# Optimization experiments

Hardware: AMD Instinct MI355X
Metric: run time of the kernel (lower is better)

The kernel has to match this reference:

```python
import jax, jax.numpy as jnp
import numpy as np

B, T, C, HEAD = 4, 4096, 1024, 64

def _rope_tables(t, d):
    # standard RoPE angles; each frequency repeated for the (even, odd) pair
    inv_freq = 1.0 / (10000.0 ** (np.arange(0, d, 2, dtype=np.float32) / d))  # (d/2,)
    ang = np.arange(t, dtype=np.float32)[:, None] * inv_freq[None, :]          # (t, d/2)
    ang = np.repeat(ang, 2, axis=-1)                                           # (t, d)
    return jnp.asarray(np.cos(ang)), jnp.asarray(np.sin(ang))

def setup_inputs() -> dict:
    key = jax.random.key(0)
    kx, kq, kk, kv = jax.random.split(key, 4)
    cos, sin = _rope_tables(T, HEAD)
    s = 1.0 / np.sqrt(C)
    return {
        "x": jax.random.normal(kx, (B, T, C), dtype=jnp.float32),
        "cos": cos,
        "sin": sin,
        "tril": jnp.tril(jnp.ones((T, T), dtype=jnp.int32)),
        "Wq": jax.random.normal(kq, (C, HEAD), dtype=jnp.float32) * s,
        "Wk": jax.random.normal(kk, (C, HEAD), dtype=jnp.float32) * s,
        "Wv": jax.random.normal(kv, (C, HEAD), dtype=jnp.float32) * s,
    }

def _apply_rope(x, cos, sin):
    # x: (B, T, D); cos/sin: (T, D)
    x1 = x[..., ::2]
    x2 = x[..., 1::2]
    rot = jnp.stack([-x2, x1], axis=-1).reshape(x.shape)
    return x * cos[None] + rot * sin[None]

def reference(x, cos, sin, tril, Wq, Wk, Wv):
    q = _apply_rope(x @ Wq, cos, sin)          # (B, T, D)
    k = _apply_rope(x @ Wk, cos, sin)          # (B, T, D)
    v = x @ Wv                                  # (B, T, D)
    scale = HEAD ** -0.5
    wei = jnp.einsum("btd,bsd->bts", q, k) * scale   # (B, T, T)
    wei = jnp.where(tril[None] == 0, -jnp.inf, wei)
    wei = jax.nn.softmax(wei, axis=-1)               # dropout p=0 (eval) -> identity
    return jnp.einsum("bts,bsd->btd", wei, v)        # (B, T, D)
```

## Files before the change

### kernel.cpp

```cpp
#include <hip/hip_runtime.h>
#include <math.h>

#define T_ 4096
#define NROWS 16384

typedef __attribute__((ext_vector_type(8))) short short8;
typedef __attribute__((ext_vector_type(4))) short short4v;
typedef __attribute__((ext_vector_type(4))) float float4v;
typedef __attribute__((ext_vector_type(2))) unsigned uint2v;

#define MFMA(a, b, c) __builtin_amdgcn_mfma_f32_16x16x32_bf16((a), (b), (c), 0, 0, 0)

#if defined(__has_builtin)
#if __has_builtin(__builtin_amdgcn_exp2f)
#define EXP2(x) __builtin_amdgcn_exp2f(x)
#else
#define EXP2(x) exp2f(x)
#endif
#else
#define EXP2(x) exp2f(x)
#endif

#define SCALE_Q 0.18033688011112042f

__device__ __forceinline__ short f2bf(float f) {
    unsigned u = __builtin_bit_cast(unsigned, f);
    u += 0x7fffu + ((u >> 16) & 1u);
    return (short)(u >> 16);
}
__device__ __forceinline__ float bf2f(short s) {
    return __builtin_bit_cast(float, ((unsigned)(unsigned short)s) << 16);
}
__device__ __forceinline__ unsigned pack_bf2(float a, float b) {
    unsigned ua = __builtin_bit_cast(unsigned, a);
    unsigned ub = __builtin_bit_cast(unsigned, b);
    ua += 0x7fffu + ((ua >> 16) & 1u);
    ub += 0x7fffu + ((ub >> 16) & 1u);
    return (ua >> 16) | (ub & 0xffff0000u);
}

__global__ void wprep_kernel(const float* __restrict__ Wq,
                             const float* __restrict__ Wk,
                             const float* __restrict__ Wv,
                             short* __restrict__ Wt2)
{
    const int ck = blockIdx.x;
    const int t = threadIdx.x;
    const int sub = t >> 6, lane = t & 63;
    const int ln = lane & 15, quad = lane >> 4;
#pragma unroll
    for (int jj = 0; jj < 3; ++jj) {
        const int nt = sub * 3 + jj;
        const float* W = (nt < 4) ? Wq : (nt < 8) ? Wk : Wv;
        const int col = (nt & 3) * 16 + ln;
        short8 o;
#pragma unroll
        for (int j = 0; j < 8; ++j)
            o[j] = f2bf(W[(size_t)(ck * 32 + quad * 8 + j) * 64 + col]);
        *(short8*)(Wt2 + ((size_t)(ck * 12 + nt) * 64 + lane) * 8) = o;
    }
}

__global__ __launch_bounds__(256, 2) void qkv_kernel(
    const float* __restrict__ x, const float* __restrict__ cosp,
    const float* __restrict__ sinp, const short* __restrict__ Wt2,
    short* __restrict__ Qb, short* __restrict__ Ks, short* __restrict__ Vs)
{
    __shared__ short4v MB[4][2][12][64];
    __shared__ short KT[32][72];

    const int t = threadIdx.x, w = t >> 6, lane = t & 63;
    const int ln = lane & 15, quad = lane >> 4;
    const int rb = blockIdx.x * 32;
    const int k0 = w * 256;

    const float* xp0 = x + (size_t)(rb + ln) * 1024 + k0 + quad * 8;
    const float* xp1 = x + (size_t)(rb + 16 + ln) * 1024 + k0 + quad * 8;
    const short* wp2 = Wt2 + ((size_t)(w * 8) * 12 * 64 + lane) * 8;

    short8 a[2][8];
#pragma unroll
    for (int af = 0; af < 2; ++af) {
        const float* xp = af ? xp1 : xp0;
        float4 xf[16];
#pragma unroll
        for (int it = 0; it < 8; ++it) {
            xf[it * 2]     = *(const float4*)(xp + it * 32);
            xf[it * 2 + 1] = *(const float4*)(xp + it * 32 + 4);
        }
#pragma unroll
        for (int it = 0; it < 8; ++it) {
            short8 v;
            v[0] = f2bf(xf[it * 2].x);     v[1] = f2bf(xf[it * 2].y);
            v[2] = f2bf(xf[it * 2].z);     v[3] = f2bf(xf[it * 2].w);
            v[4] = f2bf(xf[it * 2 + 1].x); v[5] = f2bf(xf[it * 2 + 1].y);
            v[6] = f2bf(xf[it * 2 + 1].z); v[7] = f2bf(xf[it * 2 + 1].w);
            a[af][it] = v;
        }
    }

    float4v acc[2][12];
#pragma unroll
    for (int af = 0; af < 2; ++af)
#pragma unroll
        for (int i = 0; i < 12; ++i) acc[af][i] = (float4v){0.f, 0.f, 0.f, 0.f};

#pragma unroll
    for (int it = 0; it < 8; ++it) {
        short8 bf[12];
#pragma unroll
        for (int nt = 0; nt < 12; ++nt)
            bf[nt] = *(const short8*)(wp2 + (size_t)(it * 12 + nt) * 512);
#pragma unroll
        for (int nt = 0; nt < 12; ++nt) {
            acc[0][nt] = MFMA(a[0][it], bf[nt], acc[0][nt]);
            acc[1][nt] = MFMA(a[1][it], bf[nt], acc[1][nt]);
        }
    }

#pragma unroll
    for (int af = 0; af < 2; ++af)
#pragma unroll
        for (int nt = 0; nt < 12; ++nt) {
            short4v pv;
#pragma unroll
            for (int reg = 0; reg < 4; ++reg) pv[reg] = f2bf(acc[af][nt][reg]);
            MB[w][af][nt][lane] = pv;
        }
    __syncthreads();

    const int b  = rb >> 12;
    const int kt = (rb & (T_ - 1)) >> 6;
#pragma unroll
    for (int af = 0; af < 2; ++af) {
        const int rb16 = rb + af * 16;
#pragma unroll
        for (int j = 0; j < 3; ++j) {
            const int nt = w * 3 + j;
            float m[4] = {0.f, 0.f, 0.f, 0.f};
#pragma unroll
            for (int p = 0; p < 4; ++p) {
                const short4v pv = MB[p][af][nt][lane];
#pragma unroll
                for (int reg = 0; reg < 4; ++reg) m[reg] += bf2f(pv[reg]);
            }
            if (nt < 4) {
                const int col = nt * 16 + ln;
#pragma unroll
                for (int reg = 0; reg < 4; ++reg) {
                    const int g  = rb16 + quad * 4 + reg;
                    const int tp = g & (T_ - 1);
                    const float cv = cosp[(size_t)tp * 64 + col];
                    const float sv = sinp[(size_t)tp * 64 + col];
                    const float v  = m[reg];
                    const float vp = __shfl_xor(v, 1, 64);
                    const float rot = (ln & 1) ? vp : -vp;
                    Qb[(size_t)g * 64 + col] = f2bf(fmaf(v, cv, rot * sv) * SCALE_Q);
                }
            } else if (nt < 8) {
                const int col = (nt & 3) * 16 + ln;
#pragma unroll
                for (int reg = 0; reg < 4; ++reg) {
                    const int g  = rb16 + quad * 4 + reg;
                    const int tp = g & (T_ - 1);
                    const float cv = cosp[(size_t)tp * 64 + col];
                    const float sv = sinp[(size_t)tp * 64 + col];
                    const float v  = m[reg];
                    const float vp = __shfl_xor(v, 1, 64);
                    const float rot = (ln & 1) ? vp : -vp;
                    KT[af * 16 + quad * 4 + reg][col] = f2bf(fmaf(v, cv, rot * sv));
                }
            } else {
                const int vnt = nt - 8;
                const int rowgrp = (rb16 >> 4) & 3;
                const int hh = rowgrp >> 1;
                const int qp = (rowgrp & 1) * 2 + (quad >> 1);
                const int jb = (quad & 1) * 4;
                short4v pv;
#pragma unroll
                for (int reg = 0; reg < 4; ++reg) pv[reg] = f2bf(m[reg]);
                const size_t addr =
                    ((((size_t)(b * 64 + kt) * 4 + vnt) * 2 + hh) * 64 + qp * 16 + ln) * 8 + jb;
                *(short4v*)(Vs + addr) = pv;
            }
        }
    }
    __syncthreads();

    {
        const int af2 = w >> 1, h2 = w & 1;
        const int st2 = ((rb >> 4) & 3) + af2;
        const short8 kfrag = *(const short8*)(&KT[af2 * 16 + ln][h2 * 32 + quad * 8]);
        *(short8*)(Ks + (((size_t)(b * 64 + kt) * 8 + st2 * 2 + h2) * 64 + lane) * 8) = kfrag;
    }
}

#define LOADK(kf, ktv)                                                         \
    {   const short* _kb = Ksp + (size_t)(ktv) * 4096 + lane * 8;              \
        _Pragma("unroll")                                                      \
        for (int u = 0; u < 8; ++u) kf[u] = *(const short8*)(_kb + u * 512); }

#define LOADV(vf, ktv)                                                         \
    {   const short* _vb = Vp + (size_t)(ktv) * 4096 + lane * 8;               \
        _Pragma("unroll")                                                      \
        for (int u = 0; u < 8; ++u) vf[u] = *(const short8*)(_vb + u * 512); }

#define STEP(ktv, kf, vf, masked)                                              \
    {   float4v s[4];                                                          \
        _Pragma("unroll")                                                      \
        for (int st = 0; st < 4; ++st) {                                       \
            s[st] = (float4v){0.f, 0.f, 0.f, 0.f};                             \
            s[st] = MFMA(kf[st * 2],     qb0, s[st]);         \
            s[st] = MFMA(kf[st * 2 + 1], qb1, s[st]);                          \
        }                                                                      \
        if (masked) {                                                          \
            _Pragma("unroll")                                                  \
            for (int st = 0; st < 4; ++st)                                     \
                _Pragma("unroll")                                              \
                for (int r = 0; r < 4; ++r)                                    \
                    if ((ktv) * 64 + st * 16 + quad * 4 + r > qr0 + ln)        \
                        s[st][r] = -__builtin_inff();                          \
        }                                                                      \
        _Pragma("unroll")                                                      \
        for (int st = 0; st < 4; ++st)                                         \
            _Pragma("unroll")                                                  \
            for (int r = 0; r < 4; ++r) {                                      \
                const float p = EXP2(s[st][r]);                                \
                s[st][r] = p; lsum += p;                                       \
            }                                                                  \
        _Pragma("unroll")                                                      \
        for (int st = 0; st < 4; ++st) {                                       \
            uint2v pk;                                                         \
            pk[0] = pack_bf2(s[st][0], s[st][1]);                              \
            pk[1] = pack_bf2(s[st][2], s[st][3]);                              \
            *(uint2v*)(pw + ln * 104 + st * 16 + quad * 4) = pk;               \
        }                                                                      \
        const short8 ap0 = *(const short8*)(pw + ln * 104 + quad * 8);         \
        const short8 ap1 = *(const short8*)(pw + ln * 104 + quad * 8 + 32);    \
        _Pragma("unroll")                                                      \
        for (int vn = 0; vn < 4; ++vn) {                                       \
            o[vn] = MFMA(ap0, vf[vn * 2],     o[vn]);                          \
            o[vn] = MFMA(ap1, vf[vn * 2 + 1], o[vn]);                          \
        }                                                                      \
    }

__global__ __launch_bounds__(256, 2) void attn_kernel(
    const short* __restrict__ Qb, const short* __restrict__ Ks,
    const short* __restrict__ Vs, float* __restrict__ out)
{
    __shared__ __align__(16) short PLs[4][16 * 104];
    __shared__ float OL[4][16][68];
    __shared__ float SL[4][16];

    const int t = threadIdx.x, w = t >> 6, lane = t & 63;
    const int ln = lane & 15, quad = lane >> 4;
    const int b = blockIdx.y;
    const short* Qp  = Qb + (size_t)b * T_ * 64;
    const short* Ksp = Ks + (size_t)b * T_ * 64;
    const short* Vp  = Vs + (size_t)b * T_ * 64;
    short* pw = PLs[w];

    for (int job = 0; job < 2; ++job) {
        const int qi = job ? 255 - (int)blockIdx.x : (int)blockIdx.x;
        const int qr0 = qi * 16;

        const short8 qb0 = *(const short8*)(Qp + (size_t)(qr0 + ln) * 64 + quad * 8);
        const short8 qb1 = *(const short8*)(Qp + (size_t)(qr0 + ln) * 64 + quad * 8 + 32);

        float lsum = 0.f;
        float4v o[4];
#pragma unroll
        for (int i = 0; i < 4; ++i) o[i] = (float4v){0.f, 0.f, 0.f, 0.f};

        const int ktend = qi >> 2;
        short8 k0f[8], k1f[8], v0f[8], v1f[8];

        int kt = w;
        if (kt <= ktend) {
            LOADK(k0f, kt)
            LOADV(v0f, kt)
            while (true) {
                {
                    const bool more = (kt + 4) <= ktend;
                    if (more) { LOADK(k1f, kt + 4) LOADV(v1f, kt + 4) }
                    STEP(kt, k0f, v0f, kt == ktend)
                    kt += 4;
                    if (!more) break;
                }
                {
                    const bool more = (kt + 4) <= ktend;
                    if (more) { LOADK(k0f, kt + 4) LOADV(v0f, kt + 4) }
                    STEP(kt, k1f, v1f, kt == ktend)
                    kt += 4;
                    if (!more) break;
                }
            }
        }

        lsum += __shfl_xor(lsum, 16, 64);
        lsum += __shfl_xor(lsum, 32, 64);

#pragma unroll
        for (int vn = 0; vn < 4; ++vn)
#pragma unroll
            for (int r = 0; r < 4; ++r)
                OL[w][quad * 4 + r][vn * 16 + ln] = o[vn][r];
        if (quad == 0) SL[w][ln] = lsum;
        __syncthreads();

        const int row = w * 4 + quad;
        const float lstar = SL[0][row] + SL[1][row] + SL[2][row] + SL[3][row];
        float ox = 0.f, oy = 0.f, oz = 0.f, ow = 0.f;
#pragma unroll
        for (int p = 0; p < 4; ++p) {
            const float4 ov = *(const float4*)&OL[p][row][ln * 4];
            ox += ov.x; oy += ov.y; oz += ov.z; ow += ov.w;
        }
        const float inv = 1.f / lstar;
        float4 res; res.x = ox * inv; res.y = oy * inv; res.z = oz * inv; res.w = ow * inv;
        *(float4*)(out + ((size_t)b * T_ + qr0 + row) * 64 + ln * 4) = res;
        __syncthreads();
    }
}

extern "C" void kernel_launch(void* const* d_in, const int* in_sizes, int n_in,
                              void* d_out, int out_size, void* d_ws, size_t ws_size,
                              hipStream_t stream)
{
    const float* x    = (const float*)d_in[0];
    const float* cosp = (const float*)d_in[1];
    const float* sinp = (const float*)d_in[2];
    const float* Wq   = (const float*)d_in[4];
    const float* Wk   = (const float*)d_in[5];
    const float* Wv   = (const float*)d_in[6];
    float* out = (float*)d_out;

    short* Qb  = (short*)d_ws;
    short* Ks  = Qb + (size_t)NROWS * 64;
    short* Vs  = Ks + (size_t)NROWS * 64;
    short* Wt2 = Vs + (size_t)NROWS * 64;

    wprep_kernel<<<32, 256, 0, stream>>>(Wq, Wk, Wv, Wt2);
    qkv_kernel<<<NROWS / 32, 256, 0, stream>>>(x, cosp, sinp, Wt2, Qb, Ks, Vs);
    attn_kernel<<<dim3(128, 4), 256, 0, stream>>>(Qb, Ks, Vs, out);
}
```

Measured before the change: 180.1 us.

## Process two 16-row query subtiles per wave to reuse K/V fragments

Each wave now computes attention for 32 query rows (two 16-row subtiles) against every K/V fragment it loads, so global K/V traffic per query row is halved. Blocks grow to 512 threads (8 waves striding over key tiles by 8), and the grid shrinks to 256 blocks with balanced front/back causal jobs. The P staging buffer and the cross-wave output reduction buffers now share one aliased shared-memory region, so an extra barrier is added before the reduction writes. The cost is roughly double the accumulator and score registers per wave, under a tighter launch bound of 512 threads with 2 blocks per CU, which risks register spills or lower occupancy.

Measured after the change: 187.9 us. 4.3% more time.

```diff
diff --git a/kernel.cpp b/kernel.cpp
--- a/kernel.cpp
+++ b/kernel.cpp
@@ -206,73 +206,97 @@
         for (int u = 0; u < 8; ++u) vf[u] = *(const short8*)(_vb + u * 512); }
 
 #define STEP(ktv, kf, vf, masked)                                              \
-    {   float4v s[4];                                                          \
+    {   float4v sA[4], sB[4];                                                  \
         _Pragma("unroll")                                                      \
         for (int st = 0; st < 4; ++st) {                                       \
-            s[st] = (float4v){0.f, 0.f, 0.f, 0.f};                             \
-            s[st] = MFMA(kf[st * 2],     qb0, s[st]);         \
-            s[st] = MFMA(kf[st * 2 + 1], qb1, s[st]);                          \
+            sA[st] = (float4v){0.f, 0.f, 0.f, 0.f};                            \
+            sA[st] = MFMA(kf[st * 2],     qA0, sA[st]);       \
+            sA[st] = MFMA(kf[st * 2 + 1], qA1, sA[st]);                        \
+            sB[st] = (float4v){0.f, 0.f, 0.f, 0.f};                            \
+            sB[st] = MFMA(kf[st * 2],     qB0, sB[st]);                        \
+            sB[st] = MFMA(kf[st * 2 + 1], qB1, sB[st]);                        \
         }                                                                      \
         if (masked) {                                                          \
             _Pragma("unroll")                                                  \
             for (int st = 0; st < 4; ++st)                                     \
                 _Pragma("unroll")                                              \
-                for (int r = 0; r < 4; ++r)                                    \
-                    if ((ktv) * 64 + st * 16 + quad * 4 + r > qr0 + ln)        \
-                        s[st][r] = -__builtin_inff();                          \
+                for (int r = 0; r < 4; ++r) {                                  \
+                    const int kc = (ktv) * 64 + st * 16 + quad * 4 + r;        \
+                    if (kc > qr0 + ln)      sA[st][r] = -__builtin_inff();     \
+                    if (kc > qr0 + 16 + ln) sB[st][r] = -__builtin_inff();     \
+                }                                                              \
         }                                                                      \
         _Pragma("unroll")                                                      \
         for (int st = 0; st < 4; ++st)                                         \
             _Pragma("unroll")                                                  \
             for (int r = 0; r < 4; ++r) {                                      \
-                const float p = EXP2(s[st][r]);                                \
-                s[st][r] = p; lsum += p;                                       \
+                const float pA = EXP2(sA[st][r]);                              \
+                sA[st][r] = pA; lsumA += pA;                                   \
+                const float pB = EXP2(sB[st][r]);                              \
+                sB[st][r] = pB; lsumB += pB;                                   \
             }                                                                  \
         _Pragma("unroll")                                                      \
         for (int st = 0; st < 4; ++st) {                                       \
-            uint2v pk;                                                         \
-            pk[0] = pack_bf2(s[st][0], s[st][1]);                              \
-            pk[1] = pack_bf2(s[st][2], s[st][3]);                              \
-            *(uint2v*)(pw + ln * 104 + st * 16 + quad * 4) = pk;               \
+            uint2v pkA, pkB;                                                   \
+            pkA[0] = pack_bf2(sA[st][0], sA[st][1]);                           \
+            pkA[1] = pack_bf2(sA[st][2], sA[st][3]);                           \
+            *(uint2v*)(pwA + ln * 104 + st * 16 + quad * 4) = pkA;             \
+            pkB[0] = pack_bf2(sB[st][0], sB[st][1]);                           \
+            pkB[1] = pack_bf2(sB[st][2], sB[st][3]);                           \
+            *(uint2v*)(pwB + ln * 104 + st * 16 + quad * 4) = pkB;             \
         }                                                                      \
-        const short8 ap0 = *(const short8*)(pw + ln * 104 + quad * 8);         \
-        const short8 ap1 = *(const short8*)(pw + ln * 104 + quad * 8 + 32);    \
+        const short8 aA0 = *(const short8*)(pwA + ln * 104 + quad * 8);        \
+        const short8 aA1 = *(const short8*)(pwA + ln * 104 + quad * 8 + 32);   \
+        const short8 aB0 = *(const short8*)(pwB + ln * 104 + quad * 8);        \
+        const short8 aB1 = *(const short8*)(pwB + ln * 104 + quad * 8 + 32);   \
         _Pragma("unroll")                                                      \
         for (int vn = 0; vn < 4; ++vn) {                                       \
-            o[vn] = MFMA(ap0, vf[vn * 2],     o[vn]);                          \
-            o[vn] = MFMA(ap1, vf[vn * 2 + 1], o[vn]);                          \
+            oA[vn] = MFMA(aA0, vf[vn * 2],     oA[vn]);                        \
+            oA[vn] = MFMA(aA1, vf[vn * 2 + 1], oA[vn]);                        \
+            oB[vn] = MFMA(aB0, vf[vn * 2],     oB[vn]);                        \
+            oB[vn] = MFMA(aB1, vf[vn * 2 + 1], oB[vn]);                        \
         }                                                                      \
     }
 
-__global__ __launch_bounds__(256, 2) void attn_kernel(
+__global__ __launch_bounds__(512, 2) void attn_kernel(
     const short* __restrict__ Qb, const short* __restrict__ Ks,
     const short* __restrict__ Vs, float* __restrict__ out)
 {
-    __shared__ __align__(16) short PLs[4][16 * 104];
-    __shared__ float OL[4][16][68];
-    __shared__ float SL[4][16];
+    __shared__ __align__(16) unsigned char smem[70656];
+    short* const PLs = (short*)smem;
+    float* const OLf = (float*)smem;
+    float* const SLf = (float*)(smem + 69632);
 
     const int t = threadIdx.x, w = t >> 6, lane = t & 63;
     const int ln = lane & 15, quad = lane >> 4;
-    const int b = blockIdx.y;
+    const int bid = (int)blockIdx.x;
+    const int b = bid >> 6;
+    const int q = bid & 63;
+
     const short* Qp  = Qb + (size_t)b * T_ * 64;
     const short* Ksp = Ks + (size_t)b * T_ * 64;
     const short* Vp  = Vs + (size_t)b * T_ * 64;
-    short* pw = PLs[w];
+    short* const pwA = PLs + (size_t)(w * 2) * 1664;
+    short* const pwB = pwA + 1664;
 
     for (int job = 0; job < 2; ++job) {
-        const int qi = job ? 255 - (int)blockIdx.x : (int)blockIdx.x;
-        const int qr0 = qi * 16;
-
-        const short8 qb0 = *(const short8*)(Qp + (size_t)(qr0 + ln) * 64 + quad * 8);
-        const short8 qb1 = *(const short8*)(Qp + (size_t)(qr0 + ln) * 64 + quad * 8 + 32);
-
-        float lsum = 0.f;
-        float4v o[4];
-#pragma unroll
-        for (int i = 0; i < 4; ++i) o[i] = (float4v){0.f, 0.f, 0.f, 0.f};
-
-        const int ktend = qi >> 2;
+        const int j   = job ? 127 - q : q;
+        const int qr0 = j * 32;
+
+        const short8 qA0 = *(const short8*)(Qp + (size_t)(qr0 + ln) * 64 + quad * 8);
+        const short8 qA1 = *(const short8*)(Qp + (size_t)(qr0 + ln) * 64 + quad * 8 + 32);
+        const short8 qB0 = *(const short8*)(Qp + (size_t)(qr0 + 16 + ln) * 64 + quad * 8);
+        const short8 qB1 = *(const short8*)(Qp + (size_t)(qr0 + 16 + ln) * 64 + quad * 8 + 32);
+
+        float lsumA = 0.f, lsumB = 0.f;
+        float4v oA[4], oB[4];
+#pragma unroll
+        for (int i = 0; i < 4; ++i) {
+            oA[i] = (float4v){0.f, 0.f, 0.f, 0.f};
+            oB[i] = (float4v){0.f, 0.f, 0.f, 0.f};
+        }
+
+        const int ktend = j >> 1;
         short8 k0f[8], k1f[8], v0f[8], v1f[8];
 
         int kt = w;
@@ -281,43 +305,54 @@
             LOADV(v0f, kt)
             while (true) {
                 {
-                    const bool more = (kt + 4) <= ktend;
-                    if (more) { LOADK(k1f, kt + 4) LOADV(v1f, kt + 4) }
+                    const bool more = (kt + 8) <= ktend;
+                    if (more) { LOADK(k1f, kt + 8) LOADV(v1f, kt + 8) }
                     STEP(kt, k0f, v0f, kt == ktend)
-                    kt += 4;
+                    kt += 8;
                     if (!more) break;
                 }
                 {
-                    const bool more = (kt + 4) <= ktend;
-                    if (more) { LOADK(k0f, kt + 4) LOADV(v0f, kt + 4) }
+                    const bool more = (kt + 8) <= ktend;
+                    if (more) { LOADK(k0f, kt + 8) LOADV(v0f, kt + 8) }
                     STEP(kt, k1f, v1f, kt == ktend)
-                    kt += 4;
+                    kt += 8;
                     if (!more) break;
                 }
             }
         }
 
-        lsum += __shfl_xor(lsum, 16, 64);
-        lsum += __shfl_xor(lsum, 32, 64);
+        lsumA += __shfl_xor(lsumA, 16, 64);
+        lsumA += __shfl_xor(lsumA, 32, 64);
+        lsumB += __shfl_xor(lsumB, 16, 64);
+        lsumB += __shfl_xor(lsumB, 32, 64);
+
+        __syncthreads();
 
 #pragma unroll
         for (int vn = 0; vn < 4; ++vn)
 #pragma unroll
-            for (int r = 0; r < 4; ++r)
-                OL[w][quad * 4 + r][vn * 16 + ln] = o[vn][r];
-        if (quad == 0) SL[w][ln] = lsum;
+            for (int r = 0; r < 4; ++r) {
+                OLf[((size_t)w * 32 + quad * 4 + r) * 68 + vn * 16 + ln]      = oA[vn][r];
+                OLf[((size_t)w * 32 + 16 + quad * 4 + r) * 68 + vn * 16 + ln] = oB[vn][r];
+            }
+        if (quad == 0) {
+            SLf[w * 32 + ln]      = lsumA;
+            SLf[w * 32 + 16 + ln] = lsumB;
+        }
         __syncthreads();
 
         const int row = w * 4 + quad;
-        const float lstar = SL[0][row] + SL[1][row] + SL[2][row] + SL[3][row];
-        float ox = 0.f, oy = 0.f, oz = 0.f, ow = 0.f;
-#pragma unroll
-        for (int p = 0; p < 4; ++p) {
-            const float4 ov = *(const float4*)&OL[p][row][ln * 4];
-            ox += ov.x; oy += ov.y; oz += ov.z; ow += ov.w;
+        float lstar = 0.f;
+#pragma unroll
+        for (int p = 0; p < 8; ++p) lstar += SLf[p * 32 + row];
+        float ox = 0.f, oy = 0.f, oz = 0.f, ow_ = 0.f;
+#pragma unroll
+        for (int p = 0; p < 8; ++p) {
+            const float4 ov = *(const float4*)&OLf[((size_t)p * 32 + row) * 68 + ln * 4];
+            ox += ov.x; oy += ov.y; oz += ov.z; ow_ += ov.w;
         }
         const float inv = 1.f / lstar;
-        float4 res; res.x = ox * inv; res.y = oy * inv; res.z = oz * inv; res.w = ow * inv;
+        float4 res; res.x = ox * inv; res.y = oy * inv; res.z = oz * inv; res.w = ow_ * inv;
         *(float4*)(out + ((size_t)b * T_ + qr0 + row) * 64 + ln * 4) = res;
         __syncthreads();
     }
@@ -342,5 +377,5 @@
 
     wprep_kernel<<<32, 256, 0, stream>>>(Wq, Wk, Wv, Wt2);
     qkv_kernel<<<NROWS / 32, 256, 0, stream>>>(x, cosp, sinp, Wt2, Qb, Ks, Vs);
-    attn_kernel<<<dim3(128, 4), 256, 0, stream>>>(Qb, Ks, Vs, out);
-}
+    attn_kernel<<<256, 512, 0, stream>>>(Qb, Ks, Vs, out);
+}
```
